# Optimization experiments

Measured on AMD Instinct MI355X. Metric: run time of the kernel, lower is better.

Reference implementation:

```python
import jax, jax.numpy as jnp
import numpy as np

SFREQ = 200.0
PATCH = 60
STRIDE = 30           # patch_size * (1 - overlap)
NPERSEG = min(PATCH // 2, 32)   # = 30
STEP = NPERSEG // 2   # scipy welch default noverlap = nperseg//2
NSEG = (PATCH - NPERSEG) // STEP + 1
NF = NPERSEG // 2 + 1
_w = 0.5 * (1.0 - np.cos(2.0 * np.pi * np.arange(NPERSEG) / NPERSEG))  # periodic hann (scipy default)
HANN = jnp.asarray(_w, jnp.float32)
WIN_NORM = float(SFREQ * np.sum(_w ** 2))  # density scaling
_f = np.arange(NF) * SFREQ / NPERSEG
FREQS = jnp.asarray(_f, jnp.float32)
BANDS = jnp.asarray(np.stack([((_f >= lo) & (_f <= hi)).astype(np.float32)
                              for lo, hi in [(1, 4), (4, 8), (8, 13), (13, 30), (30, 99)]]), jnp.float32)
ONESIDED = jnp.asarray(np.concatenate([[1.0], 2.0 * np.ones(NF - 2), [1.0]]), jnp.float32)


def layer_norm(v, g, b, eps=1e-5):
    mu = v.mean(-1, keepdims=True)
    var = ((v - mu) ** 2).mean(-1, keepdims=True)
    return (v - mu) * jax.lax.rsqrt(var + eps) * g + b


def features(p):
    # p: (B, P, PATCH)
    L = p.shape[-1]
    mx = p.max(-1); mn = p.min(-1); mean = p.mean(-1)
    c = p - mean[..., None]
    m2 = (c ** 2).mean(-1); m3 = (c ** 3).mean(-1); m4 = (c ** 4).mean(-1)
    std = jnp.sqrt(m2)
    peak_loc = jnp.argmax(jnp.abs(p), -1).astype(jnp.float32) / L
    dx = jnp.diff(p, axis=-1)
    zc = jnp.sum(jnp.diff(jnp.sign(p + 1e-10), axis=-1) != 0, axis=-1).astype(jnp.float32) / L
    kurt = m4 / (m2 ** 2) - 3.0   # scipy Fisher, biased
    skew = m3 / (m2 ** 1.5)
    morph = jnp.stack([mx, mn, mx - mn, mean, std, peak_loc,
                       dx.max(-1), dx.min(-1), jnp.abs(dx).mean(-1),
                       zc, (p ** 2).sum(-1), kurt, skew], -1)
    morph = jnp.where(jnp.isfinite(morph), morph, 0.0)
    # Welch PSD (detrend='constant', hann, density, one-sided, mean over segments)
    seg_idx = jnp.arange(NSEG)[:, None] * STEP + jnp.arange(NPERSEG)
    segs = p[..., seg_idx]                             # (B,P,NSEG,NPERSEG)
    segs = (segs - segs.mean(-1, keepdims=True)) * HANN
    X = jnp.fft.rfft(segs, axis=-1)                    # (B,P,NSEG,NF)
    psd = ((X.real ** 2 + X.imag ** 2) / WIN_NORM * ONESIDED).mean(-2)  # (B,P,NF)
    total = psd.sum(-1) + 1e-12
    bandp = jnp.einsum('bpf,kf->bpk', psd, BANDS) / total[..., None]
    peakf = FREQS[jnp.argmax(psd, -1)]
    cs = jnp.cumsum(psd, -1)
    edge = FREQS[jnp.argmax(cs >= 0.95 * total[..., None], -1)]
    pn = psd / total[..., None]
    ent = -jnp.sum(pn * jnp.log2(pn + 1e-12), -1)
    spec = jnp.concatenate([bandp, jnp.stack([peakf, edge, ent, total], -1)], -1)
    spec = jnp.where(jnp.isfinite(spec), spec, 0.0)
    return morph, spec


def setup_inputs() -> dict:
    key = jax.random.key(0)
    ks = jax.random.split(key, 8)
    B, T, E = 1024, 6000, 256
    n_m, n_s = 13, 9
    nf = n_m + n_s
    x = jax.random.normal(ks[0], (B, 1, T), jnp.float32)
    return {
        'x': x,
        'g_m': jnp.ones((n_m,), jnp.float32), 'b_m': jnp.zeros((n_m,), jnp.float32),
        'g_s': jnp.ones((n_s,), jnp.float32), 'b_s': jnp.zeros((n_s,), jnp.float32),
        'W1': jax.random.normal(ks[1], (nf, E // 2), jnp.float32) * 0.05,
        'b1': jnp.zeros((E // 2,), jnp.float32),
        'W2': jax.random.normal(ks[2], (E // 2, E), jnp.float32) * 0.05,
        'b2': jnp.zeros((E,), jnp.float32),
        'g_o': jnp.ones((E,), jnp.float32), 'b_o': jnp.zeros((E,), jnp.float32),
    }


def reference(x, g_m, b_m, g_s, b_s, W1, b1, W2, b2, g_o, b_o):
    B, _, T = x.shape
    n_patches = (T - PATCH) // STRIDE + 1
    idx = jnp.arange(n_patches)[:, None] * STRIDE + jnp.arange(PATCH)
    p = x[:, 0, :][:, idx]                     # (B, n_patches, PATCH)
    morph, spec = features(p)
    combined = jnp.concatenate([layer_norm(morph, g_m, b_m), layer_norm(spec, g_s, b_s)], -1)
    h = jax.nn.gelu(combined @ W1 + b1, approximate=False)  # dropout = identity (eval)
    return layer_norm(h @ W2 + b2, g_o, b_o)   # (B, n_patches, emb_size)
```

## Files before the change

### kernel.cpp

```cpp
#include <hip/hip_runtime.h>
#include <math.h>

#define NPERSEG 30
#define STEPW 15
#define NSEG 3
#define NF 16
#define PATCH 60
#define STRIDE 30
#define NP_ROW 199
#define NBATCH 1024
#define T_LEN 6000
#define NPATCH_TOTAL (NBATCH * NP_ROW)
#define GB 32
#define NBLK_B (NPATCH_TOTAL / GB)

constexpr double TC[30] = {
  1.0,
  0.97814760073380563793,
  0.91354545764260089550,
  0.80901699437494742410,
  0.66913060635885821383,
  0.5,
  0.30901699437494742410,
  0.10452846326765347140,
 -0.10452846326765347140,
 -0.30901699437494742410,
 -0.5,
 -0.66913060635885821383,
 -0.80901699437494742410,
 -0.91354545764260089550,
 -0.97814760073380563793,
 -1.0,
 -0.97814760073380563793,
 -0.91354545764260089550,
 -0.80901699437494742410,
 -0.66913060635885821383,
 -0.5,
 -0.30901699437494742410,
 -0.10452846326765347140,
  0.10452846326765347140,
  0.30901699437494742410,
  0.5,
  0.66913060635885821383,
  0.80901699437494742410,
  0.91354545764260089550,
  0.97814760073380563793,
};
constexpr double TS[30] = {
  0.0,
  0.20791169081775933710,
  0.40673664307580020775,
  0.58778525229247312917,
  0.74314482547739423501,
  0.86602540378443864676,
  0.95105651629515357212,
  0.99452189536827333692,
  0.99452189536827333692,
  0.95105651629515357212,
  0.86602540378443864676,
  0.74314482547739423501,
  0.58778525229247312917,
  0.40673664307580020775,
  0.20791169081775933710,
  0.0,
 -0.20791169081775933710,
 -0.40673664307580020775,
 -0.58778525229247312917,
 -0.74314482547739423501,
 -0.86602540378443864676,
 -0.95105651629515357212,
 -0.99452189536827333692,
 -0.99452189536827333692,
 -0.95105651629515357212,
 -0.86602540378443864676,
 -0.74314482547739423501,
 -0.58778525229247312917,
 -0.40673664307580020775,
 -0.20791169081775933710,
};
constexpr double INV_WN = 1.0 / 2250.0;
constexpr double THIRD  = 1.0 / 3.0;

__device__ __forceinline__ float np_sum30_f32(const float* a) {
    float r[8];
#pragma unroll
    for (int j = 0; j < 8; ++j) r[j] = a[j];
#pragma unroll
    for (int i = 8; i < 24; i += 8)
#pragma unroll
        for (int j = 0; j < 8; ++j) r[j] += a[i + j];
    float res = ((r[0] + r[1]) + (r[2] + r[3])) + ((r[4] + r[5]) + (r[6] + r[7]));
#pragma unroll
    for (int i = 24; i < 30; ++i) res += a[i];
    return res;
}

__device__ __forceinline__ double np_sum16_f64(const double* a) {
    double r[8];
#pragma unroll
    for (int j = 0; j < 8; ++j) r[j] = a[j] + a[8 + j];
    return ((r[0] + r[1]) + (r[2] + r[3])) + ((r[4] + r[5]) + (r[6] + r[7]));
}

__global__ __launch_bounds__(256) void feat_kernel(
    const float* __restrict__ x,
    const float* __restrict__ g_m, const float* __restrict__ b_m,
    const float* __restrict__ g_s, const float* __restrict__ b_s,
    float* __restrict__ out)
{
    __shared__ float xs[T_LEN];

    const int tid = threadIdx.x;
    const int row = blockIdx.x;

    {
        const float4* src = reinterpret_cast<const float4*>(x + (size_t)row * T_LEN);
        float4* dst = reinterpret_cast<float4*>(xs);
        for (int i = tid; i < T_LEN / 4; i += 256) dst[i] = src[i];
    }
    __syncthreads();
    if (tid >= NP_ROW) return;

    const float* pf = xs + tid * STRIDE;
    float f[22];

    double morph[13];
    {
        double vmax = (double)pf[0], vmin = vmax, vsum = 0.0;
#pragma unroll
        for (int n = 0; n < PATCH; ++n) {
            double v = (double)pf[n];
            vmax = fmax(vmax, v); vmin = fmin(vmin, v); vsum += v;
        }
        double vmean = vsum / 60.0;
        double s2 = 0.0, s3 = 0.0, s4 = 0.0, ssq = 0.0;
#pragma unroll
        for (int n = 0; n < PATCH; ++n) {
            double v = (double)pf[n];
            double c = v - vmean, c2 = c * c;
            s2 += c2; s3 += c2 * c; s4 += c2 * c2;
            ssq += v * v;
        }
        double m2 = s2 / 60.0, m3 = s3 / 60.0, m4 = s4 / 60.0;
        double vstd = sqrt(m2);

        int amax = 0; float aval = fabsf(pf[0]);
#pragma unroll
        for (int n = 1; n < PATCH; ++n) {
            float a = fabsf(pf[n]);
            if (a > aval) { aval = a; amax = n; }
        }
        double peak_loc = (double)((float)amax / 60.0f);

        double dmax = (double)pf[1] - (double)pf[0], dmin = dmax, dabssum = 0.0;
#pragma unroll
        for (int n = 0; n < PATCH - 1; ++n) {
            double d = (double)pf[n + 1] - (double)pf[n];
            dmax = fmax(dmax, d); dmin = fmin(dmin, d); dabssum += fabs(d);
        }
        double dabsmean = dabssum / 59.0;

        int zc = 0;
        {
            float v0 = pf[0] + 1e-10f;
            int prev = (v0 > 0.0f) - (v0 < 0.0f);
#pragma unroll
            for (int n = 1; n < PATCH; ++n) {
                float v = pf[n] + 1e-10f;
                int s = (v > 0.0f) - (v < 0.0f);
                if (s != prev) zc++;
                prev = s;
            }
        }
        double zcf = (double)zc / 60.0;
        double kurt = m4 / (m2 * m2) - 3.0;
        double skew = m3 / (m2 * sqrt(m2));

        morph[0] = vmax;  morph[1] = vmin;  morph[2] = vmax - vmin;
        morph[3] = vmean; morph[4] = vstd;  morph[5] = peak_loc;
        morph[6] = dmax;  morph[7] = dmin;  morph[8] = dabsmean;
        morph[9] = zcf;   morph[10] = ssq;  morph[11] = kurt; morph[12] = skew;
#pragma unroll
        for (int i = 0; i < 13; ++i) if (!isfinite(morph[i])) morph[i] = 0.0;
    }
    {
        double mu = 0.0;
#pragma unroll
        for (int i = 0; i < 13; ++i) mu += morph[i];
        mu /= 13.0;
        double var = 0.0;
#pragma unroll
        for (int i = 0; i < 13; ++i) { double d = morph[i] - mu; var += d * d; }
        var /= 13.0;
        double inv = 1.0 / sqrt(var + 1e-5);
#pragma unroll
        for (int i = 0; i < 13; ++i)
            f[i] = (float)((morph[i] - mu) * inv * (double)g_m[i] + (double)b_m[i]);
    }

    double psd[NF];
#pragma unroll
    for (int k = 0; k < NF; ++k) psd[k] = 0.0;

#pragma unroll 1
    for (int s = 0; s < NSEG; ++s) {
        float q[NPERSEG];
#pragma unroll
        for (int n = 0; n < NPERSEG; ++n) q[n] = pf[s * STEPW + n];

        float res = np_sum30_f32(q);
        float smean = res / 30.0f;
        float y[NPERSEG];
#pragma unroll
        for (int n = 0; n < NPERSEG; ++n) {
            const float hn = (float)(0.5 * (1.0 - TC[n]));
            y[n] = (q[n] - smean) * hn;
        }

        double y0  = (double)y[0];
        double y15 = (double)y[15];
        double u[15], v[15];
#pragma unroll
        for (int m = 1; m < 15; ++m) {
            double a = (double)y[m], b = (double)y[NPERSEG - m];
            u[m] = a + b;
            v[m] = a - b;
        }

#pragma unroll
        for (int k = 0; k < NF; ++k) {
            double re = (k & 1) ? (y0 - y15) : (y0 + y15);
            double im = 0.0;
#pragma unroll
            for (int m = 1; m < 15; ++m) {
                const double tcv = TC[(k * m) % 30];
                const double tsv = TS[(k * m) % 30];
                re += u[m] * tcv;
                if (tsv != 0.0) im += v[m] * tsv;
            }
            double pw = re * re + im * im;
            pw *= INV_WN;
            if (k != 0 && k != NF - 1) pw = pw + pw;
            psd[k] += pw;
        }
    }
#pragma unroll
    for (int k = 0; k < NF; ++k) psd[k] = psd[k] * THIRD;

    double total = np_sum16_f64(psd) + 1e-12;
    double invt = 1.0 / total;

    double band1 = psd[1] * invt;
    double band3 = ((psd[2] + psd[3]) + psd[4]) * invt;
    double b4s = 0.0;
#pragma unroll
    for (int k = 5; k <= 14; ++k) b4s += psd[k];
    double band4 = b4s * invt;

    int bk = 0; double bpv = psd[0];
#pragma unroll
    for (int k = 1; k < NF; ++k) if (psd[k] > bpv) { bpv = psd[k]; bk = k; }

    double th = 0.95 * total;
    int ek = 0;
    {
        double acc = 0.0; bool found = false;
#pragma unroll
        for (int k = 0; k < NF; ++k) {
            acc += psd[k];
            if (!found && acc >= th) { ek = k; found = true; }
        }
    }

    double ent = 0.0;
#pragma unroll
    for (int k = 0; k < NF; ++k) {
        double pn = psd[k] * invt;
        ent -= pn * log2(pn + 1e-12);
    }

    double spec[9];
    spec[0] = 0.0;
    spec[1] = band1;
    spec[2] = 0.0;
    spec[3] = band3;
    spec[4] = band4;
    spec[5] = (double)((float)((double)bk * 200.0 / 30.0));
    spec[6] = (double)((float)((double)ek * 200.0 / 30.0));
    spec[7] = ent;
    spec[8] = total;
#pragma unroll
    for (int i = 0; i < 9; ++i) if (!isfinite(spec[i])) spec[i] = 0.0;

    {
        double mu = 0.0;
#pragma unroll
        for (int i = 0; i < 9; ++i) mu += spec[i];
        mu /= 9.0;
        double var = 0.0;
#pragma unroll
        for (int i = 0; i < 9; ++i) { double d = spec[i] - mu; var += d * d; }
        var /= 9.0;
        double inv = 1.0 / sqrt(var + 1e-5);
#pragma unroll
        for (int i = 0; i < 9; ++i)
            f[13 + i] = (float)((spec[i] - mu) * inv * (double)g_s[i] + (double)b_s[i]);
    }

    const int p = row * NP_ROW + tid;
    float* op = out + (size_t)(p >> 5) * (GB * 256) + (size_t)(p & 31) * 22;
#pragma unroll
    for (int i = 0; i < 11; ++i)
        *reinterpret_cast<float2*>(op + 2 * i) = make_float2(f[2 * i], f[2 * i + 1]);
}

__global__ __launch_bounds__(256, 4) void mlp_kernel(
    const float* __restrict__ W1, const float* __restrict__ b1,
    const float* __restrict__ W2, const float* __restrict__ b2,
    const float* __restrict__ g_o, const float* __restrict__ b_o,
    float* __restrict__ out)
{
    __shared__ float Fsl[GB * 22];
    __shared__ float Hs[GB][128];

    const int tid = threadIdx.x;
    const size_t base = (size_t)blockIdx.x * (GB * 256);

    if (tid < 176)
        reinterpret_cast<float4*>(Fsl)[tid] =
            *reinterpret_cast<const float4*>(out + base + 4 * (size_t)tid);
    __syncthreads();

    {
        const int hc  = tid & 127;
        const int ppb = tid >> 7;
        float w1c[22];
#pragma unroll
        for (int k = 0; k < 22; ++k) w1c[k] = W1[k * 128 + hc];
        const float b1v = b1[hc];
#pragma unroll
        for (int v = 0; v < 16; ++v) {
            const int pp = ppb + 2 * v;
            float a = b1v;
#pragma unroll
            for (int k = 0; k < 22; ++k) a += Fsl[pp * 22 + k] * w1c[k];
            Hs[pp][hc] = 0.5f * a * (1.0f + erff(a * 0.70710678118654752440f));
        }
    }
    __syncthreads();

    const int cb = tid & 63;
    const int wv = tid >> 6;

    float4 acc[8];
    {
        const float4 b2v = *reinterpret_cast<const float4*>(b2 + 4 * cb);
#pragma unroll
        for (int p = 0; p < 8; ++p) acc[p] = b2v;
    }

#pragma unroll 2
    for (int k = 0; k < 128; k += 4) {
        float4 w0 = *reinterpret_cast<const float4*>(&W2[(k + 0) * 256 + 4 * cb]);
        float4 w1 = *reinterpret_cast<const float4*>(&W2[(k + 1) * 256 + 4 * cb]);
        float4 w2 = *reinterpret_cast<const float4*>(&W2[(k + 2) * 256 + 4 * cb]);
        float4 w3 = *reinterpret_cast<const float4*>(&W2[(k + 3) * 256 + 4 * cb]);
#pragma unroll
        for (int p = 0; p < 8; ++p) {
            const float4 h = *reinterpret_cast<const float4*>(&Hs[8 * wv + p][k]);
            acc[p].x += h.x * w0.x; acc[p].y += h.x * w0.y;
            acc[p].z += h.x * w0.z; acc[p].w += h.x * w0.w;
            acc[p].x += h.y * w1.x; acc[p].y += h.y * w1.y;
            acc[p].z += h.y * w1.z; acc[p].w += h.y * w1.w;
            acc[p].x += h.z * w2.x; acc[p].y += h.z * w2.y;
            acc[p].z += h.z * w2.z; acc[p].w += h.z * w2.w;
            acc[p].x += h.w * w3.x; acc[p].y += h.w * w3.y;
            acc[p].z += h.w * w3.z; acc[p].w += h.w * w3.w;
        }
    }

    const float4 go4 = *reinterpret_cast<const float4*>(g_o + 4 * cb);
    const float4 bo4 = *reinterpret_cast<const float4*>(b_o + 4 * cb);
#pragma unroll
    for (int p = 0; p < 8; ++p) {
        float s = (acc[p].x + acc[p].y) + (acc[p].z + acc[p].w);
        float q = (acc[p].x * acc[p].x + acc[p].y * acc[p].y)
                + (acc[p].z * acc[p].z + acc[p].w * acc[p].w);
        for (int off = 32; off; off >>= 1) {
            s += __shfl_xor(s, off);
            q += __shfl_xor(q, off);
        }
        const float mu  = s * (1.0f / 256.0f);
        const float var = q * (1.0f / 256.0f) - mu * mu;
        const float inv = rsqrtf(var + 1e-5f);
        float4 o;
        o.x = (acc[p].x - mu) * inv * go4.x + bo4.x;
        o.y = (acc[p].y - mu) * inv * go4.y + bo4.y;
        o.z = (acc[p].z - mu) * inv * go4.z + bo4.z;
        o.w = (acc[p].w - mu) * inv * go4.w + bo4.w;
        *reinterpret_cast<float4*>(out + base + (size_t)(8 * wv + p) * 256 + 4 * cb) = o;
    }
}

extern "C" void kernel_launch(void* const* d_in, const int* in_sizes, int n_in,
                              void* d_out, int out_size, void* d_ws, size_t ws_size,
                              hipStream_t stream) {
    const float* x   = (const float*)d_in[0];
    const float* g_m = (const float*)d_in[1];
    const float* b_m = (const float*)d_in[2];
    const float* g_s = (const float*)d_in[3];
    const float* b_s = (const float*)d_in[4];
    const float* W1  = (const float*)d_in[5];
    const float* b1  = (const float*)d_in[6];
    const float* W2  = (const float*)d_in[7];
    const float* b2  = (const float*)d_in[8];
    const float* g_o = (const float*)d_in[9];
    const float* b_o = (const float*)d_in[10];
    float* out = (float*)d_out;

    feat_kernel<<<NBATCH, 256, 0, stream>>>(x, g_m, b_m, g_s, b_s, out);
    mlp_kernel<<<NBLK_B, 256, 0, stream>>>(W1, b1, W2, b2, g_o, b_o, out);
}
```

Baseline: 509.9 us.

## Fuse feature loops, split DFT into halves, and retile MLP second GEMM

The feature kernel now computes max/min/sum, argmax, zero crossings and diffs in one pass, and writes the morphological features early to shorten register live ranges. The per-segment DFT drops the symmetric u/v folding and computes frequency bins in two groups of eight over all 30 samples, to reduce simultaneous double-precision register pressure at the cost of more FMAs. The MLP's second GEMM is retiled so each lane handles 8 channels for 4 patches instead of 4 channels for 8, which changes the ratio of W2 loads to Hs loads and uses a 32-lane layernorm reduction. Accumulation order changes slightly, so numerics may shift a little.

```diff
diff --git a/kernel.cpp b/kernel.cpp
--- a/kernel.cpp
+++ b/kernel.cpp
@@ -122,59 +122,53 @@
     if (tid >= NP_ROW) return;
 
     const float* pf = xs + tid * STRIDE;
-    float f[22];
+    const int p = row * NP_ROW + tid;
+    float* op = out + (size_t)(p >> 5) * (GB * 256) + (size_t)(p & 31) * 22;
 
     double morph[13];
     {
-        double vmax = (double)pf[0], vmin = vmax, vsum = 0.0;
+        const float v0f = pf[0];
+        const double v0 = (double)v0f;
+        double vmax = v0, vmin = v0, vsum = v0;
+        float aval = fabsf(v0f); int amax = 0;
+        float sv0 = v0f + 1e-10f;
+        int prev = (sv0 > 0.0f) - (sv0 < 0.0f);
+        int zc = 0;
+        double dmax = 0.0, dmin = 0.0, dabssum = 0.0;
+        double vprev = v0;
+#pragma unroll
+        for (int n = 1; n < PATCH; ++n) {
+            const float vf = pf[n];
+            const double v = (double)vf;
+            vmax = fmax(vmax, v); vmin = fmin(vmin, v); vsum += v;
+            const float a = fabsf(vf);
+            if (a > aval) { aval = a; amax = n; }
+            const float sv = vf + 1e-10f;
+            const int sg = (sv > 0.0f) - (sv < 0.0f);
+            if (sg != prev) zc++;
+            prev = sg;
+            const double d = v - vprev;
+            if (n == 1) { dmax = d; dmin = d; dabssum = fabs(d); }
+            else { dmax = fmax(dmax, d); dmin = fmin(dmin, d); dabssum += fabs(d); }
+            vprev = v;
+        }
+        const double vmean = vsum / 60.0;
+        const double dabsmean = dabssum / 59.0;
+        const double peak_loc = (double)((float)amax / 60.0f);
+        const double zcf = (double)zc / 60.0;
+
+        double s2 = 0.0, s3 = 0.0, s4 = 0.0, ssq = 0.0;
 #pragma unroll
         for (int n = 0; n < PATCH; ++n) {
-            double v = (double)pf[n];
-            vmax = fmax(vmax, v); vmin = fmin(vmin, v); vsum += v;
-        }
-        double vmean = vsum / 60.0;
-        double s2 = 0.0, s3 = 0.0, s4 = 0.0, ssq = 0.0;
-#pragma unroll
-        for (int n = 0; n < PATCH; ++n) {
-            double v = (double)pf[n];
-            double c = v - vmean, c2 = c * c;
+            const double v = (double)pf[n];
+            const double c = v - vmean, c2 = c * c;
             s2 += c2; s3 += c2 * c; s4 += c2 * c2;
             ssq += v * v;
         }
-        double m2 = s2 / 60.0, m3 = s3 / 60.0, m4 = s4 / 60.0;
-        double vstd = sqrt(m2);
-
-        int amax = 0; float aval = fabsf(pf[0]);
-#pragma unroll
-        for (int n = 1; n < PATCH; ++n) {
-            float a = fabsf(pf[n]);
-            if (a > aval) { aval = a; amax = n; }
-        }
-        double peak_loc = (double)((float)amax / 60.0f);
-
-        double dmax = (double)pf[1] - (double)pf[0], dmin = dmax, dabssum = 0.0;
-#pragma unroll
-        for (int n = 0; n < PATCH - 1; ++n) {
-            double d = (double)pf[n + 1] - (double)pf[n];
-            dmax = fmax(dmax, d); dmin = fmin(dmin, d); dabssum += fabs(d);
-        }
-        double dabsmean = dabssum / 59.0;
-
-        int zc = 0;
-        {
-            float v0 = pf[0] + 1e-10f;
-            int prev = (v0 > 0.0f) - (v0 < 0.0f);
-#pragma unroll
-            for (int n = 1; n < PATCH; ++n) {
-                float v = pf[n] + 1e-10f;
-                int s = (v > 0.0f) - (v < 0.0f);
-                if (s != prev) zc++;
-                prev = s;
-            }
-        }
-        double zcf = (double)zc / 60.0;
-        double kurt = m4 / (m2 * m2) - 3.0;
-        double skew = m3 / (m2 * sqrt(m2));
+        const double m2 = s2 / 60.0, m3 = s3 / 60.0, m4 = s4 / 60.0;
+        const double vstd = sqrt(m2);
+        const double kurt = m4 / (m2 * m2) - 3.0;
+        const double skew = m3 / (m2 * sqrt(m2));
 
         morph[0] = vmax;  morph[1] = vmin;  morph[2] = vmax - vmin;
         morph[3] = vmean; morph[4] = vstd;  morph[5] = peak_loc;
@@ -192,11 +186,18 @@
 #pragma unroll
         for (int i = 0; i < 13; ++i) { double d = morph[i] - mu; var += d * d; }
         var /= 13.0;
-        double inv = 1.0 / sqrt(var + 1e-5);
+        const double inv = 1.0 / sqrt(var + 1e-5);
+        float fm[13];
 #pragma unroll
         for (int i = 0; i < 13; ++i)
-            f[i] = (float)((morph[i] - mu) * inv * (double)g_m[i] + (double)b_m[i]);
-    }
+            fm[i] = (float)((morph[i] - mu) * inv * (double)g_m[i] + (double)b_m[i]);
+#pragma unroll
+        for (int i = 0; i < 6; ++i)
+            *reinterpret_cast<float2*>(op + 2 * i) = make_float2(fm[2 * i], fm[2 * i + 1]);
+        op[12] = fm[12];
+    }
+
+    asm volatile("" ::: "memory");
 
     double psd[NF];
 #pragma unroll
@@ -204,64 +205,86 @@
 
 #pragma unroll 1
     for (int s = 0; s < NSEG; ++s) {
-        float q[NPERSEG];
-#pragma unroll
-        for (int n = 0; n < NPERSEG; ++n) q[n] = pf[s * STEPW + n];
-
-        float res = np_sum30_f32(q);
-        float smean = res / 30.0f;
         float y[NPERSEG];
-#pragma unroll
-        for (int n = 0; n < NPERSEG; ++n) {
-            const float hn = (float)(0.5 * (1.0 - TC[n]));
-            y[n] = (q[n] - smean) * hn;
-        }
-
-        double y0  = (double)y[0];
-        double y15 = (double)y[15];
-        double u[15], v[15];
-#pragma unroll
-        for (int m = 1; m < 15; ++m) {
-            double a = (double)y[m], b = (double)y[NPERSEG - m];
-            u[m] = a + b;
-            v[m] = a - b;
-        }
-
-#pragma unroll
-        for (int k = 0; k < NF; ++k) {
-            double re = (k & 1) ? (y0 - y15) : (y0 + y15);
-            double im = 0.0;
-#pragma unroll
-            for (int m = 1; m < 15; ++m) {
-                const double tcv = TC[(k * m) % 30];
-                const double tsv = TS[(k * m) % 30];
-                re += u[m] * tcv;
-                if (tsv != 0.0) im += v[m] * tsv;
-            }
-            double pw = re * re + im * im;
-            pw *= INV_WN;
-            if (k != 0 && k != NF - 1) pw = pw + pw;
-            psd[k] += pw;
+        {
+            float q[NPERSEG];
+#pragma unroll
+            for (int n = 0; n < NPERSEG; ++n) q[n] = pf[s * STEPW + n];
+            const float res = np_sum30_f32(q);
+            const float smean = res / 30.0f;
+#pragma unroll
+            for (int n = 0; n < NPERSEG; ++n) {
+                const float hn = (float)(0.5 * (1.0 - TC[n]));
+                y[n] = (q[n] - smean) * hn;
+            }
+        }
+
+        {
+            double re[8], im[8];
+#pragma unroll
+            for (int j = 0; j < 8; ++j) { re[j] = 0.0; im[j] = 0.0; }
+#pragma unroll
+            for (int m = 0; m < NPERSEG; ++m) {
+                const double yd = (double)y[m];
+#pragma unroll
+                for (int j = 0; j < 8; ++j) {
+                    const double tcv = TC[(j * m) % 30];
+                    const double tsv = TS[(j * m) % 30];
+                    re[j] += yd * tcv;
+                    if (tsv != 0.0) im[j] += yd * tsv;
+                }
+            }
+#pragma unroll
+            for (int j = 0; j < 8; ++j) {
+                double pw = re[j] * re[j] + im[j] * im[j];
+                pw *= INV_WN;
+                if (j != 0) pw = pw + pw;
+                psd[j] += pw;
+            }
+        }
+        {
+            double re[8], im[8];
+#pragma unroll
+            for (int j = 0; j < 8; ++j) { re[j] = 0.0; im[j] = 0.0; }
+#pragma unroll
+            for (int m = 0; m < NPERSEG; ++m) {
+                const double yd = (double)y[m];
+#pragma unroll
+                for (int j = 0; j < 8; ++j) {
+                    const int k = 8 + j;
+                    const double tcv = TC[(k * m) % 30];
+                    const double tsv = TS[(k * m) % 30];
+                    re[j] += yd * tcv;
+                    if (tsv != 0.0) im[j] += yd * tsv;
+                }
+            }
+#pragma unroll
+            for (int j = 0; j < 8; ++j) {
+                double pw = re[j] * re[j] + im[j] * im[j];
+                pw *= INV_WN;
+                if (j != 7) pw = pw + pw;
+                psd[8 + j] += pw;
+            }
         }
     }
 #pragma unroll
     for (int k = 0; k < NF; ++k) psd[k] = psd[k] * THIRD;
 
-    double total = np_sum16_f64(psd) + 1e-12;
-    double invt = 1.0 / total;
-
-    double band1 = psd[1] * invt;
-    double band3 = ((psd[2] + psd[3]) + psd[4]) * invt;
+    const double total = np_sum16_f64(psd) + 1e-12;
+    const double invt = 1.0 / total;
+
+    const double band1 = psd[1] * invt;
+    const double band3 = ((psd[2] + psd[3]) + psd[4]) * invt;
     double b4s = 0.0;
 #pragma unroll
     for (int k = 5; k <= 14; ++k) b4s += psd[k];
-    double band4 = b4s * invt;
+    const double band4 = b4s * invt;
 
     int bk = 0; double bpv = psd[0];
 #pragma unroll
     for (int k = 1; k < NF; ++k) if (psd[k] > bpv) { bpv = psd[k]; bk = k; }
 
-    double th = 0.95 * total;
+    const double th = 0.95 * total;
     int ek = 0;
     {
         double acc = 0.0; bool found = false;
@@ -275,7 +298,7 @@
     double ent = 0.0;
 #pragma unroll
     for (int k = 0; k < NF; ++k) {
-        double pn = psd[k] * invt;
+        const double pn = psd[k] * invt;
         ent -= pn * log2(pn + 1e-12);
     }
 
@@ -301,17 +324,16 @@
 #pragma unroll
         for (int i = 0; i < 9; ++i) { double d = spec[i] - mu; var += d * d; }
         var /= 9.0;
-        double inv = 1.0 / sqrt(var + 1e-5);
+        const double inv = 1.0 / sqrt(var + 1e-5);
+        float fs[9];
 #pragma unroll
         for (int i = 0; i < 9; ++i)
-            f[13 + i] = (float)((spec[i] - mu) * inv * (double)g_s[i] + (double)b_s[i]);
-    }
-
-    const int p = row * NP_ROW + tid;
-    float* op = out + (size_t)(p >> 5) * (GB * 256) + (size_t)(p & 31) * 22;
-#pragma unroll
-    for (int i = 0; i < 11; ++i)
-        *reinterpret_cast<float2*>(op + 2 * i) = make_float2(f[2 * i], f[2 * i + 1]);
+            fs[i] = (float)((spec[i] - mu) * inv * (double)g_s[i] + (double)b_s[i]);
+        op[13] = fs[0];
+#pragma unroll
+        for (int i = 0; i < 4; ++i)
+            *reinterpret_cast<float2*>(op + 14 + 2 * i) = make_float2(fs[1 + 2 * i], fs[2 + 2 * i]);
+    }
 }
 
 __global__ __launch_bounds__(256, 4) void mlp_kernel(
@@ -349,56 +371,78 @@
     }
     __syncthreads();
 
-    const int cb = tid & 63;
-    const int wv = tid >> 6;
-
-    float4 acc[8];
-    {
-        const float4 b2v = *reinterpret_cast<const float4*>(b2 + 4 * cb);
-#pragma unroll
-        for (int p = 0; p < 8; ++p) acc[p] = b2v;
+    const int lane  = tid & 63;
+    const int wv    = tid >> 6;
+    const int half  = lane >> 5;
+    const int l5    = lane & 31;
+    const int ch0   = l5 * 8;
+    const int pbase = 8 * wv + 4 * half;
+
+    float4 accA[4], accB[4];
+    {
+        const float4 b2lo = *reinterpret_cast<const float4*>(b2 + ch0);
+        const float4 b2hi = *reinterpret_cast<const float4*>(b2 + ch0 + 4);
+#pragma unroll
+        for (int pp = 0; pp < 4; ++pp) { accA[pp] = b2lo; accB[pp] = b2hi; }
     }
 
 #pragma unroll 2
     for (int k = 0; k < 128; k += 4) {
-        float4 w0 = *reinterpret_cast<const float4*>(&W2[(k + 0) * 256 + 4 * cb]);
-        float4 w1 = *reinterpret_cast<const float4*>(&W2[(k + 1) * 256 + 4 * cb]);
-        float4 w2 = *reinterpret_cast<const float4*>(&W2[(k + 2) * 256 + 4 * cb]);
-        float4 w3 = *reinterpret_cast<const float4*>(&W2[(k + 3) * 256 + 4 * cb]);
-#pragma unroll
-        for (int p = 0; p < 8; ++p) {
-            const float4 h = *reinterpret_cast<const float4*>(&Hs[8 * wv + p][k]);
-            acc[p].x += h.x * w0.x; acc[p].y += h.x * w0.y;
-            acc[p].z += h.x * w0.z; acc[p].w += h.x * w0.w;
-            acc[p].x += h.y * w1.x; acc[p].y += h.y * w1.y;
-            acc[p].z += h.y * w1.z; acc[p].w += h.y * w1.w;
-            acc[p].x += h.z * w2.x; acc[p].y += h.z * w2.y;
-            acc[p].z += h.z * w2.z; acc[p].w += h.z * w2.w;
-            acc[p].x += h.w * w3.x; acc[p].y += h.w * w3.y;
-            acc[p].z += h.w * w3.z; acc[p].w += h.w * w3.w;
-        }
-    }
-
-    const float4 go4 = *reinterpret_cast<const float4*>(g_o + 4 * cb);
-    const float4 bo4 = *reinterpret_cast<const float4*>(b_o + 4 * cb);
-#pragma unroll
-    for (int p = 0; p < 8; ++p) {
-        float s = (acc[p].x + acc[p].y) + (acc[p].z + acc[p].w);
-        float q = (acc[p].x * acc[p].x + acc[p].y * acc[p].y)
-                + (acc[p].z * acc[p].z + acc[p].w * acc[p].w);
-        for (int off = 32; off; off >>= 1) {
+        float4 h[4];
+#pragma unroll
+        for (int pp = 0; pp < 4; ++pp)
+            h[pp] = *reinterpret_cast<const float4*>(&Hs[pbase + pp][k]);
+        float4 wlo[4], whi[4];
+#pragma unroll
+        for (int kk = 0; kk < 4; ++kk) {
+            wlo[kk] = *reinterpret_cast<const float4*>(&W2[(k + kk) * 256 + ch0]);
+            whi[kk] = *reinterpret_cast<const float4*>(&W2[(k + kk) * 256 + ch0 + 4]);
+        }
+#pragma unroll
+        for (int kk = 0; kk < 4; ++kk) {
+#pragma unroll
+            for (int pp = 0; pp < 4; ++pp) {
+                const float hv = (kk == 0) ? h[pp].x : (kk == 1) ? h[pp].y
+                               : (kk == 2) ? h[pp].z : h[pp].w;
+                accA[pp].x += hv * wlo[kk].x; accA[pp].y += hv * wlo[kk].y;
+                accA[pp].z += hv * wlo[kk].z; accA[pp].w += hv * wlo[kk].w;
+                accB[pp].x += hv * whi[kk].x; accB[pp].y += hv * whi[kk].y;
+                accB[pp].z += hv * whi[kk].z; accB[pp].w += hv * whi[kk].w;
+            }
+        }
+    }
+
+    const float4 golo = *reinterpret_cast<const float4*>(g_o + ch0);
+    const float4 gohi = *reinterpret_cast<const float4*>(g_o + ch0 + 4);
+    const float4 bolo = *reinterpret_cast<const float4*>(b_o + ch0);
+    const float4 bohi = *reinterpret_cast<const float4*>(b_o + ch0 + 4);
+#pragma unroll
+    for (int pp = 0; pp < 4; ++pp) {
+        float s = ((accA[pp].x + accA[pp].y) + (accA[pp].z + accA[pp].w))
+                + ((accB[pp].x + accB[pp].y) + (accB[pp].z + accB[pp].w));
+        float q = ((accA[pp].x * accA[pp].x + accA[pp].y * accA[pp].y)
+                +  (accA[pp].z * accA[pp].z + accA[pp].w * accA[pp].w))
+                + ((accB[pp].x * accB[pp].x + accB[pp].y * accB[pp].y)
+                +  (accB[pp].z * accB[pp].z + accB[pp].w * accB[pp].w));
+        for (int off = 16; off; off >>= 1) {
             s += __shfl_xor(s, off);
             q += __shfl_xor(q, off);
         }
         const float mu  = s * (1.0f / 256.0f);
         const float var = q * (1.0f / 256.0f) - mu * mu;
         const float inv = rsqrtf(var + 1e-5f);
-        float4 o;
-        o.x = (acc[p].x - mu) * inv * go4.x + bo4.x;
-        o.y = (acc[p].y - mu) * inv * go4.y + bo4.y;
-        o.z = (acc[p].z - mu) * inv * go4.z + bo4.z;
-        o.w = (acc[p].w - mu) * inv * go4.w + bo4.w;
-        *reinterpret_cast<float4*>(out + base + (size_t)(8 * wv + p) * 256 + 4 * cb) = o;
+        float4 oA, oB;
+        oA.x = (accA[pp].x - mu) * inv * golo.x + bolo.x;
+        oA.y = (accA[pp].y - mu) * inv * golo.y + bolo.y;
+        oA.z = (accA[pp].z - mu) * inv * golo.z + bolo.z;
+        oA.w = (accA[pp].w - mu) * inv * golo.w + bolo.w;
+        oB.x = (accB[pp].x - mu) * inv * gohi.x + bohi.x;
+        oB.y = (accB[pp].y - mu) * inv * gohi.y + bohi.y;
+        oB.z = (accB[pp].z - mu) * inv * gohi.z + bohi.z;
+        oB.w = (accB[pp].w - mu) * inv * gohi.w + bohi.w;
+        float* orow = out + base + (size_t)(pbase + pp) * 256 + ch0;
+        *reinterpret_cast<float4*>(orow)     = oA;
+        *reinterpret_cast<float4*>(orow + 4) = oB;
     }
 }
 
```

After: 481.0 us. 1.06x faster.
